# Kernel optimization log

Measured on AMD Instinct MI355X. Metric: run time of the kernel, lower is better.

Reference implementation:

```python
import jax, jax.numpy as jnp
import numpy as np
import math


def _strided_value_mask(L, S, dtype):
    # mask_line[L + d] == 0 when |d| is a power-of-two stride in {2,4,...,<=L};
    # value_mask[i, j] = mask_line[L - i + j], i.e. zero where |j - i| is such a stride.
    diff = jnp.abs(jnp.arange(L)[:, None] - jnp.arange(S)[None, :])  # [L, S]
    vm = jnp.ones((L, S), dtype=dtype)
    stride = 2
    while stride <= L:
        vm = vm * (diff != stride).astype(dtype)
        stride *= 2
    return vm


def setup_inputs() -> dict:
    key = jax.random.key(0)
    k1, k2, k3 = jax.random.split(key, 3)
    B, L, H, E = 4, 2048, 8, 64
    D = 64
    return {
        "queries": jax.random.normal(k1, (B, L, H, E), dtype=jnp.float32),
        "keys": jax.random.normal(k2, (B, L, H, E), dtype=jnp.float32),
        "values": jax.random.normal(k3, (B, L, H, D), dtype=jnp.float32),
    }


def reference(queries, keys, values):
    B, L, H, E = queries.shape
    S = keys.shape[1]
    scale = 1.0 / math.sqrt(E)

    # raw scores [B, H, L, S]
    scores = jnp.einsum("blhe,bshe->bhls", queries, keys)
    # multiplicative strided mask (zeroes scores at power-of-two offsets)
    vm = _strided_value_mask(L, S, scores.dtype)  # [L, S]
    scores = scores * vm
    # causal mask: upper triangle -> -inf (mask_flag=True, attn_mask=None path)
    causal = jnp.triu(jnp.ones((L, S), dtype=bool), k=1)
    scores = jnp.where(causal, -jnp.inf, scores)

    # dropout p=0.0 (eval) -> identity
    A = jax.nn.softmax(scale * scores, axis=-1)
    V = jnp.einsum("bhls,bshd->blhd", A, values)
    return V
```

## Files before the change

### kernel.cpp

```cpp
#include <hip/hip_runtime.h>
#include <hip/hip_bf16.h>
#include <stdint.h>

typedef __attribute__((ext_vector_type(8))) short short8;
typedef __attribute__((ext_vector_type(16))) float f32x16;

namespace {
constexpr int NB = 4, NL = 2048, NH = 8, NE = 64, ND = 64;
constexpr float KS = 0.125f * 1.44269504f;
constexpr int NCHUNK = 40;
constexpr int RECSZ  = 8320;
constexpr int KSTEP  = 64 * NH * NE;
}

__device__ const unsigned char TG[40] = {
  3,7,7,10,11,11,11,14,14,15,15,15,15,
  6,6,9,9,10,10,12,12,13,13,13,13,14,14,
  2,5,5,8,8,8,9,12,12,
  4,4,1,0};
__device__ const unsigned char TT0[40] = {
  0,0,16,0,0,16,32,0,16,0,16,32,48,
  0,14,0,14,16,30,0,14,0,14,28,42,32,46,
  0,0,12,0,12,24,28,28,40,
  0,10,0,0};
__device__ const unsigned char TT1[40] = {
  16,16,32,16,16,32,48,16,32,16,32,48,64,
  14,28,14,28,30,44,14,28,14,28,42,56,46,60,
  12,12,24,12,24,36,40,40,52,
  10,20,8,4};
__device__ const unsigned char TREC[40] = {
  3,10,11,18,21,22,23,32,33,36,37,38,39,
  8,9,15,16,19,20,24,25,28,29,30,31,34,35,
  2,6,7,12,13,14,17,26,27,
  4,5,1,0};
__device__ const unsigned char CUMD[16] = {0,1,2,3,4,6,8,10,12,15,18,21,24,28,32,36};
__device__ const unsigned char NCHD[16] = {1,1,1,1,2,2,2,2,3,3,3,3,4,4,4,4};

__device__ __forceinline__ ushort bfb(float x) {
  __hip_bfloat16 b(x);
  return __builtin_bit_cast(ushort, b);
}
__device__ __forceinline__ uint32_t pkbf(float lo, float hi) {
  return (uint32_t)bfb(lo) | ((uint32_t)bfb(hi) << 16);
}

#define LD(RR) do {                                                         \
    const float* kp_ = kpp + (size_t)(RR) * KSTEP;                          \
    const float* vp_ = vpp + (size_t)(RR) * KSTEP;                          \
    kx0 = *(const float4*)(kp_);      kx1 = *(const float4*)(kp_ + 4);      \
    kx2 = *(const float4*)(kp_ + 8);  kx3 = *(const float4*)(kp_ + 12);     \
    vx0 = *(const float4*)(vp_);               vx1 = *(const float4*)(vp_ + NH*ND); \
    vx2 = *(const float4*)(vp_ + 2*NH*ND);     vx3 = *(const float4*)(vp_ + 3*NH*ND); \
  } while (0)

#define STG() do {                                                          \
    uint4 kwA = { pkbf(kx0.x,kx0.y), pkbf(kx0.z,kx0.w),                     \
                  pkbf(kx1.x,kx1.y), pkbf(kx1.z,kx1.w) };                   \
    uint4 kwB = { pkbf(kx2.x,kx2.y), pkbf(kx2.z,kx2.w),                     \
                  pkbf(kx3.x,kx3.y), pkbf(kx3.z,kx3.w) };                   \
    *(uint4*)((char*)lds.kt + krow*128 + ( kcol2        ^ kswz)) = kwA;     \
    *(uint4*)((char*)lds.kt + krow*128 + ((kcol2 + 16)  ^ kswz)) = kwB;     \
    _Pragma("unroll")                                                       \
    for (int j_ = 0; j_ < 4; ++j_) {                                        \
      int d_ = vd0 + j_;                                                    \
      char* vr_ = (char*)lds.vt + d_*128;                                   \
      int vs_ = (d_ & 7) << 4;                                              \
      *(uint32_t*)(vr_ + ((vk0*2    ) ^ vs_)) = pkbf(vx0[j_], vx1[j_]);     \
      *(uint32_t*)(vr_ + ((vk0*2 + 4) ^ vs_)) = pkbf(vx2[j_], vx3[j_]);     \
    }                                                                       \
  } while (0)

#define COMPUTE(TT, SUB) do {                                               \
    const int kv0_ = (TT) * 32;                                             \
    f32x16 s;                                                               \
    _Pragma("unroll")                                                       \
    for (int i_ = 0; i_ < 16; ++i_) s[i_] = 0.f;                            \
    { const char* kb_ = (const char*)lds.kt + ((SUB)*32 + ln31) * 128;      \
      _Pragma("unroll")                                                     \
      for (int st_ = 0; st_ < 4; ++st_) {                                   \
        short8 kf_ = *(const short8*)(kb_ + ((st_*32 + hi*16) ^ rsw));      \
        s = __builtin_amdgcn_mfma_f32_32x32x16_bf16(kf_, qf[st_], s, 0,0,0);\
      } }                                                                   \
    const int delta_ = q0w - kv0_;                                          \
    const int qrelh_ = (qi - kv0_) - 4 * hi;                                \
    if ((TT) == tw) {                          \
      _Pragma("unroll")                                                     \
      for (int r_ = 0; r_ < 16; ++r_) {                                     \
        const int cr_ = (r_ & 3) + 8 * (r_ >> 2);                           \
        int diff_ = qrelh_ - cr_;                                           \
        float lg_ = s[r_];                                                  \
        bool p2_ = (diff_ > 1) & ((diff_ & (diff_ - 1)) == 0);              \
        lg_ = p2_ ? 0.f : lg_;                                              \
        lg_ = (diff_ < 0) ? -__builtin_inff() : lg_;                        \
        s[r_] = exp2f(lg_);                                                 \
      }                                                                     \
    } else {                                                                \
      int pmax_ = 1 << (31 - __clz(delta_ + 31));                           \
      if (pmax_ >= delta_ - 31) {        \
        _Pragma("unroll")                                                   \
        for (int r_ = 0; r_ < 16; ++r_) {                                   \
          const int cr_ = (r_ & 3) + 8 * (r_ >> 2);                         \
          int diff_ = qrelh_ - cr_;                                         \
          bool p2_ = (diff_ > 1) & ((diff_ & (diff_ - 1)) == 0);            \
          s[r_] = exp2f(p2_ ? 0.f : s[r_]);                                 \
        }                                                                   \
      } else {                                        \
        _Pragma("unroll")                                                   \
        for (int r_ = 0; r_ < 16; ++r_) s[r_] = exp2f(s[r_]);               \
      }                                                                     \
    }                                                                       \
    uint32_t w0_ = pkbf(s[0],  s[1]),  w1_ = pkbf(s[2],  s[3]);             \
    uint32_t w2_ = pkbf(s[4],  s[5]),  w3_ = pkbf(s[6],  s[7]);             \
    uint32_t w4_ = pkbf(s[8],  s[9]),  w5_ = pkbf(s[10], s[11]);            \
    uint32_t w6_ = pkbf(s[12], s[13]), w7_ = pkbf(s[14], s[15]);            \
    uint32_t y0_ = __shfl_xor(hi ? w0_ : w2_, 32);                          \
    uint32_t y1_ = __shfl_xor(hi ? w1_ : w3_, 32);                          \
    uint32_t y2_ = __shfl_xor(hi ? w4_ : w6_, 32);                          \
    uint32_t y3_ = __shfl_xor(hi ? w5_ : w7_, 32);                          \
    union { short8 v; uint32_t u[4]; } f0_, f1_;                            \
    if (hi == 0) {                                                          \
      f0_.u[0] = w0_; f0_.u[1] = w1_; f0_.u[2] = y0_; f0_.u[3] = y1_;       \
      f1_.u[0] = w4_; f1_.u[1] = w5_; f1_.u[2] = y2_; f1_.u[3] = y3_;       \
    } else {                                                                \
      f0_.u[0] = y0_; f0_.u[1] = y1_; f0_.u[2] = w2_; f0_.u[3] = w3_;       \
      f1_.u[0] = y2_; f1_.u[1] = y3_; f1_.u[2] = w6_; f1_.u[3] = w7_;       \
    }                                                                       \
    { const char* vb_ = (const char*)lds.vt;                                \
      const char* vr0_ = vb_ + ln31 * 128;                                  \
      const char* vr1_ = vb_ + (32 + ln31) * 128;                           \
      short8 a00_ = *(const short8*)(vr0_ + (((SUB)*64      + hi*16) ^ rsw));\
      short8 a01_ = *(const short8*)(vr0_ + (((SUB)*64 + 32 + hi*16) ^ rsw));\
      short8 a10_ = *(const short8*)(vr1_ + (((SUB)*64      + hi*16) ^ rsw));\
      short8 a11_ = *(const short8*)(vr1_ + (((SUB)*64 + 32 + hi*16) ^ rsw));\
      acc0 = __builtin_amdgcn_mfma_f32_32x32x16_bf16(a00_, f0_.v, acc0, 0,0,0); \
      acc0 = __builtin_amdgcn_mfma_f32_32x32x16_bf16(a01_, f1_.v, acc0, 0,0,0); \
      acc1 = __builtin_amdgcn_mfma_f32_32x32x16_bf16(a10_, f0_.v, acc1, 0,0,0); \
      acc1 = __builtin_amdgcn_mfma_f32_32x32x16_bf16(a11_, f1_.v, acc1, 0,0,0); \
      accl = __builtin_amdgcn_mfma_f32_32x32x16_bf16(onesv, f0_.v, accl, 0,0,0);\
      accl = __builtin_amdgcn_mfma_f32_32x32x16_bf16(onesv, f1_.v, accl, 0,0,0);\
    }                                                                       \
  } while (0)

__global__ __launch_bounds__(256, 3)
void sattn_part(const float* __restrict__ Qg, const float* __restrict__ Kg,
                const float* __restrict__ Vg, float* __restrict__ W)
{
  const int id = blockIdx.x;
  const int bh = id & 31;
  const int e  = id >> 5;
  const int g  = TG[e];
  const int t0 = TT0[e], t1 = TT1[e];
  float* rec = W + (size_t)(bh * NCHUNK + TREC[e]) * RECSZ;
  const int b = bh >> 3, h = bh & 7;

  const int tid  = threadIdx.x;
  const int wave = tid >> 6;
  const int lane = tid & 63;
  const int ln31 = lane & 31;
  const int hi   = lane >> 5;

  __shared__ __align__(16) struct { ushort kt[64 * 64]; ushort vt[64 * 64]; } lds;

  const int q0w = g * 128 + wave * 32;
  const int qi  = q0w + ln31;
  const int tw  = 4 * g + wave;

  short8 qf[4];
  {
    const float* qp = Qg + (((size_t)b * NL + qi) * NH + h) * NE;
    #pragma unroll
    for (int st = 0; st < 4; ++st) {
      const float* qpe = qp + st * 16 + hi * 8;
      union { short8 v; uint32_t u[4]; } f;
      #pragma unroll
      for (int j = 0; j < 4; ++j)
        f.u[j] = pkbf(qpe[2 * j] * KS, qpe[2 * j + 1] * KS);
      qf[st] = f.v;
    }
  }
  short8 onesv;
  {
    union { short8 v; uint32_t u[4]; } o;
    #pragma unroll
    for (int j = 0; j < 4; ++j) o.u[j] = 0x3F803F80u;
    onesv = o.v;
  }

  f32x16 acc0, acc1, accl;
  #pragma unroll
  for (int i = 0; i < 16; ++i) { acc0[i] = 0.f; acc1[i] = 0.f; accl[i] = 0.f; }

  const int krow = tid >> 2,        kcol = (tid & 3) * 16;
  const int vk0  = (tid & 15) * 4,  vd0  = (tid >> 4) * 4;
  const int kbase = t0 * 32;
  const float* kpp = Kg + (((size_t)b * NL + kbase + krow) * NH + h) * NE + kcol;
  const float* vpp = Vg + (((size_t)b * NL + kbase + vk0 ) * NH + h) * ND + vd0;

  const int kswz  = (krow & 7) << 4;
  const int kcol2 = kcol * 2;
  const int rsw   = (ln31 & 7) << 4;

  float4 kx0, kx1, kx2, kx3, vx0, vx1, vx2, vx3;

  const int nr = (t1 - t0) >> 1;
  LD(0);
  STG();
  __syncthreads();
  if (nr > 1) LD(1);
  for (int r = 0;;) {
    const int tt = t0 + 2 * r;
    if (tt     <= tw) COMPUTE(tt,     0);
    if (tt + 1 <= tw) COMPUTE(tt + 1, 1);
    if (++r == nr) break;
    __syncthreads();
    STG();
    __syncthreads();
    if (r + 1 < nr) LD(r + 1);
  }

  #pragma unroll
  for (int r = 0; r < 16; ++r) {
    int d = (r & 3) + 8 * (r >> 2) + 4 * hi;
    rec[d * 128 + wave * 32 + ln31]        = acc0[r];
    rec[(32 + d) * 128 + wave * 32 + ln31] = acc1[r];
  }
  if (hi == 0) rec[8192 + wave * 32 + ln31] = accl[0];
}

__global__ __launch_bounds__(256)
void sattn_combine(const float* __restrict__ W, float* __restrict__ Og)
{
  const int id = blockIdx.x;
  const int h2 = id & 1, g = (id >> 1) & 15, bh = id >> 5;
  const int b = bh >> 3, h = bh & 7;
  const int tid = threadIdx.x;

  __shared__ float sd[64][67];
  __shared__ float Lq[64];

  const float* rec0 = W + (size_t)(bh * NCHUNK + CUMD[g]) * RECSZ;
  const int nc = NCHD[g];

  #pragma unroll
  for (int rep = 0; rep < 4; ++rep) {
    int d  = rep * 16 + (tid >> 4);
    int q4 = (tid & 15) * 4;
    float4 a = {0.f, 0.f, 0.f, 0.f};
    for (int c = 0; c < nc; ++c) {
      float4 v = *(const float4*)(rec0 + (size_t)c * RECSZ + d * 128 + h2 * 64 + q4);
      a.x += v.x; a.y += v.y; a.z += v.z; a.w += v.w;
    }
    sd[d][q4 + 0] = a.x; sd[d][q4 + 1] = a.y;
    sd[d][q4 + 2] = a.z; sd[d][q4 + 3] = a.w;
  }
  if (tid < 64) {
    float a = 0.f;
    for (int c = 0; c < nc; ++c) a += rec0[(size_t)c * RECSZ + 8192 + h2 * 64 + tid];
    Lq[tid] = 1.0f / a;
  }
  __syncthreads();
  #pragma unroll
  for (int rep = 0; rep < 4; ++rep) {
    int q  = rep * 16 + (tid >> 4);
    int d4 = (tid & 15) * 4;
    float l = Lq[q];
    float4 o = { sd[d4][q] * l, sd[d4 + 1][q] * l, sd[d4 + 2][q] * l, sd[d4 + 3][q] * l };
    *(float4*)(Og + (((size_t)b * NL + g * 128 + h2 * 64 + q) * NH + h) * ND + d4) = o;
  }
}

__global__ __launch_bounds__(256)
void sattn_mono(const float* __restrict__ Qg, const float* __restrict__ Kg,
                const float* __restrict__ Vg, float* __restrict__ Og)
{
  const int bh = blockIdx.x;
  const int y  = blockIdx.y;
  const int qblk = (y < 8) ? (15 - y) : (y - 8);
  const int b = bh >> 3, h = bh & 7;
  const int tid  = threadIdx.x;
  const int wave = tid >> 6;
  const int lane = tid & 63;
  const int ln31 = lane & 31;
  const int hi   = lane >> 5;

  __shared__ __align__(16) union {
    struct { ushort kt[32 * 64]; ushort vt[64 * 40]; } s;
    float ep[4 * 32 * 68];
  } lds;

  const int q0w = qblk * 128 + wave * 32;
  const int qi  = q0w + ln31;
  const int tw  = qblk * 4 + wave;
  const int NT  = qblk * 4 + 4;

  short8 qf[4];
  {
    const float* qp = Qg + (((size_t)b * NL + qi) * NH + h) * NE;
    #pragma unroll
    for (int st = 0; st < 4; ++st) {
      const float* qpe = qp + st * 16 + hi * 8;
      union { short8 v; uint32_t u[4]; } f;
      #pragma unroll
      for (int j = 0; j < 4; ++j) f.u[j] = pkbf(qpe[2 * j] * KS, qpe[2 * j + 1] * KS);
      qf[st] = f.v;
    }
  }
  f32x16 acc0, acc1;
  #pragma unroll
  for (int i = 0; i < 16; ++i) { acc0[i] = 0.f; acc1[i] = 0.f; }
  float ls = 0.f;

  const int krow = tid >> 3,        kcol = (tid & 7) * 8;
  const int vrow = (tid >> 4) * 2,  vcol = (tid & 15) * 4;
  const float* kpp = Kg + (((size_t)b * NL + krow) * NH + h) * NE + kcol;
  const float* vpp = Vg + (((size_t)b * NL + vrow) * NH + h) * ND + vcol;
  constexpr int KS32 = 32 * NH * NE;

  float kx[8], vx[8];
  #pragma unroll
  for (int j = 0; j < 8; ++j) kx[j] = kpp[j];
  #pragma unroll
  for (int j = 0; j < 4; ++j) { vx[j] = vpp[j]; vx[4 + j] = vpp[j + NH * ND]; }

  for (int t = 0; t < NT; ++t) {
    const int kv0 = t * 32;
    __syncthreads();
    {
      uint32_t* kd = (uint32_t*)((char*)lds.s.kt + krow * 128 +
                                 ((kcol * 2) ^ ((krow & 7) << 4)));
      kd[0] = pkbf(kx[0], kx[1]); kd[1] = pkbf(kx[2], kx[3]);
      kd[2] = pkbf(kx[4], kx[5]); kd[3] = pkbf(kx[6], kx[7]);
      #pragma unroll
      for (int j = 0; j < 4; ++j) {
        int d = vcol + j;
        *(uint32_t*)((char*)lds.s.vt + d * 80 +
                     ((vrow * 2) ^ (((d >> 3) & 3) << 4))) = pkbf(vx[j], vx[4 + j]);
      }
    }
    {
      int tn = (t + 1 < NT) ? t + 1 : t;
      const float* kp = kpp + (size_t)tn * KS32;
      const float* vp = vpp + (size_t)tn * KS32;
      #pragma unroll
      for (int j = 0; j < 8; ++j) kx[j] = kp[j];
      #pragma unroll
      for (int j = 0; j < 4; ++j) { vx[j] = vp[j]; vx[4 + j] = vp[j + NH * ND]; }
    }
    __syncthreads();
    if (t > tw) continue;

    f32x16 s;
    #pragma unroll
    for (int i = 0; i < 16; ++i) s[i] = 0.f;
    const char* kb  = (const char*)lds.s.kt + ln31 * 128;
    const int   ksw = (ln31 & 7) << 4;
    #pragma unroll
    for (int st = 0; st < 4; ++st) {
      short8 kf = *(const short8*)(kb + ((st * 32 + hi * 16) ^ ksw));
      s = __builtin_amdgcn_mfma_f32_32x32x16_bf16(kf, qf[st], s, 0, 0, 0);
    }
    const int delta = q0w - kv0;
    const int qrelh = (qi - kv0) - 4 * hi;
    float ps = 0.f;
    if (t == tw) {
      #pragma unroll
      for (int r = 0; r < 16; ++r) {
        const int cr = (r & 3) + 8 * (r >> 2);
        int diff = qrelh - cr;
        float lg = s[r];
        bool p2 = (diff > 1) & ((diff & (diff - 1)) == 0);
        lg = p2 ? 0.f : lg;
        lg = (diff < 0) ? -__builtin_inff() : lg;
        float p = exp2f(lg); s[r] = p; ps += p;
      }
    } else {
      int pmax = 1 << (31 - __clz(delta + 31));
      if (pmax >= delta - 31) {
        #pragma unroll
        for (int r = 0; r < 16; ++r) {
          const int cr = (r & 3) + 8 * (r >> 2);
          int diff = qrelh - cr;
          bool p2 = (diff > 1) & ((diff & (diff - 1)) == 0);
          float p = exp2f(p2 ? 0.f : s[r]); s[r] = p; ps += p;
        }
      } else {
        #pragma unroll
        for (int r = 0; r < 16; ++r) { float p = exp2f(s[r]); s[r] = p; ps += p; }
      }
    }
    ls += ps;

    uint32_t w0 = pkbf(s[0],  s[1]),  w1 = pkbf(s[2],  s[3]);
    uint32_t w2 = pkbf(s[4],  s[5]),  w3 = pkbf(s[6],  s[7]);
    uint32_t w4 = pkbf(s[8],  s[9]),  w5 = pkbf(s[10], s[11]);
    uint32_t w6 = pkbf(s[12], s[13]), w7 = pkbf(s[14], s[15]);
    uint32_t y0 = __shfl_xor(hi ? w0 : w2, 32);
    uint32_t y1 = __shfl_xor(hi ? w1 : w3, 32);
    uint32_t y2 = __shfl_xor(hi ? w4 : w6, 32);
    uint32_t y3 = __shfl_xor(hi ? w5 : w7, 32);
    union { short8 v; uint32_t u[4]; } f0, f1;
    if (hi == 0) {
      f0.u[0] = w0; f0.u[1] = w1; f0.u[2] = y0; f0.u[3] = y1;
      f1.u[0] = w4; f1.u[1] = w5; f1.u[2] = y2; f1.u[3] = y3;
    } else {
      f0.u[0] = y0; f0.u[1] = y1; f0.u[2] = w2; f0.u[3] = w3;
      f1.u[0] = y2; f1.u[1] = y3; f1.u[2] = w6; f1.u[3] = w7;
    }
    const char* vb = (const char*)lds.s.vt;
    const int d0 = ln31,      sw0 = ((d0 >> 3) & 3) << 4;
    const int d1 = 32 + ln31, sw1 = ((d1 >> 3) & 3) << 4;
    short8 a00 = *(const short8*)(vb + d0 * 80 + ((hi * 16) ^ sw0));
    short8 a01 = *(const short8*)(vb + d0 * 80 + ((32 + hi * 16) ^ sw0));
    short8 a10 = *(const short8*)(vb + d1 * 80 + ((hi * 16) ^ sw1));
    short8 a11 = *(const short8*)(vb + d1 * 80 + ((32 + hi * 16) ^ sw1));
    acc0 = __builtin_amdgcn_mfma_f32_32x32x16_bf16(a00, f0.v, acc0, 0, 0, 0);
    acc0 = __builtin_amdgcn_mfma_f32_32x32x16_bf16(a01, f1.v, acc0, 0, 0, 0);
    acc1 = __builtin_amdgcn_mfma_f32_32x32x16_bf16(a10, f0.v, acc1, 0, 0, 0);
    acc1 = __builtin_amdgcn_mfma_f32_32x32x16_bf16(a11, f1.v, acc1, 0, 0, 0);
  }

  __syncthreads();
  ls += __shfl_xor(ls, 32);
  const float inv = 1.0f / ls;
  float* ep = lds.ep + wave * (32 * 68);
  #pragma unroll
  for (int r = 0; r < 16; ++r) {
    int drow = (r & 3) + 8 * (r >> 2) + 4 * hi;
    ep[ln31 * 68 + drow]      = acc0[r] * inv;
    ep[ln31 * 68 + 32 + drow] = acc1[r] * inv;
  }
  __syncthreads();
  const float* epr = lds.ep + wave * (32 * 68);
  #pragma unroll
  for (int rep = 0; rep < 8; ++rep) {
    int q  = rep * 4 + (lane >> 4);
    int d4 = (lane & 15) * 4;
    float4 val = *(const float4*)(epr + q * 68 + d4);
    float* op = Og + (((size_t)b * NL + q0w + q) * NH + h) * ND + d4;
    *(float4*)op = val;
  }
}

extern "C" void kernel_launch(void* const* d_in, const int* in_sizes, int n_in,
                              void* d_out, int out_size, void* d_ws, size_t ws_size,
                              hipStream_t stream) {
  const float* Q = (const float*)d_in[0];
  const float* K = (const float*)d_in[1];
  const float* V = (const float*)d_in[2];
  float* O = (float*)d_out;
  const size_t need = (size_t)32 * NCHUNK * RECSZ * sizeof(float);
  if (ws_size >= need) {
    sattn_part<<<dim3(32 * NCHUNK), dim3(256), 0, stream>>>(Q, K, V, (float*)d_ws);
    sattn_combine<<<dim3(1024), dim3(256), 0, stream>>>((const float*)d_ws, O);
  } else {
    sattn_mono<<<dim3(32, 16), dim3(256), 0, stream>>>(Q, K, V, O);
  }
}
```

Before: 65.49 us.

## Double-buffer K/V tiles in LDS to drop one barrier per iteration

Splits the shared-memory K/V staging area into two ping-pong buffers so the next tile can be written while the current one is read. This removes one of the two __syncthreads per iteration. The global load for the next tile is now issued before compute, and the launch bound is raised to 4 blocks per CU. LDS use doubles to 32KB per block, and the added occupancy target may limit registers and cause spills.

```diff
diff --git a/kernel.cpp b/kernel.cpp
--- a/kernel.cpp
+++ b/kernel.cpp
@@ -53,29 +53,29 @@
     vx2 = *(const float4*)(vp_ + 2*NH*ND);     vx3 = *(const float4*)(vp_ + 3*NH*ND); \
   } while (0)
 
-#define STG() do {                                                          \
+#define STG(KB, VB) do {                                                    \
     uint4 kwA = { pkbf(kx0.x,kx0.y), pkbf(kx0.z,kx0.w),                     \
                   pkbf(kx1.x,kx1.y), pkbf(kx1.z,kx1.w) };                   \
     uint4 kwB = { pkbf(kx2.x,kx2.y), pkbf(kx2.z,kx2.w),                     \
                   pkbf(kx3.x,kx3.y), pkbf(kx3.z,kx3.w) };                   \
-    *(uint4*)((char*)lds.kt + krow*128 + ( kcol2        ^ kswz)) = kwA;     \
-    *(uint4*)((char*)lds.kt + krow*128 + ((kcol2 + 16)  ^ kswz)) = kwB;     \
+    *(uint4*)((KB) + krow*128 + ( kcol2        ^ kswz)) = kwA;              \
+    *(uint4*)((KB) + krow*128 + ((kcol2 + 16)  ^ kswz)) = kwB;              \
     _Pragma("unroll")                                                       \
     for (int j_ = 0; j_ < 4; ++j_) {                                        \
       int d_ = vd0 + j_;                                                    \
-      char* vr_ = (char*)lds.vt + d_*128;                                   \
+      char* vr_ = (VB) + d_*128;                                            \
       int vs_ = (d_ & 7) << 4;                                              \
       *(uint32_t*)(vr_ + ((vk0*2    ) ^ vs_)) = pkbf(vx0[j_], vx1[j_]);     \
       *(uint32_t*)(vr_ + ((vk0*2 + 4) ^ vs_)) = pkbf(vx2[j_], vx3[j_]);     \
     }                                                                       \
   } while (0)
 
-#define COMPUTE(TT, SUB) do {                                               \
+#define COMPUTE(TT, SUB, KB, VB) do {                                       \
     const int kv0_ = (TT) * 32;                                             \
     f32x16 s;                                                               \
     _Pragma("unroll")                                                       \
     for (int i_ = 0; i_ < 16; ++i_) s[i_] = 0.f;                            \
-    { const char* kb_ = (const char*)lds.kt + ((SUB)*32 + ln31) * 128;      \
+    { const char* kb_ = (const char*)(KB) + ((SUB)*32 + ln31) * 128;        \
       _Pragma("unroll")                                                     \
       for (int st_ = 0; st_ < 4; ++st_) {                                   \
         short8 kf_ = *(const short8*)(kb_ + ((st_*32 + hi*16) ^ rsw));      \
@@ -125,9 +125,8 @@
       f0_.u[0] = y0_; f0_.u[1] = y1_; f0_.u[2] = w2_; f0_.u[3] = w3_;       \
       f1_.u[0] = y2_; f1_.u[1] = y3_; f1_.u[2] = w6_; f1_.u[3] = w7_;       \
     }                                                                       \
-    { const char* vb_ = (const char*)lds.vt;                                \
-      const char* vr0_ = vb_ + ln31 * 128;                                  \
-      const char* vr1_ = vb_ + (32 + ln31) * 128;                           \
+    { const char* vr0_ = (const char*)(VB) + ln31 * 128;                    \
+      const char* vr1_ = (const char*)(VB) + (32 + ln31) * 128;             \
       short8 a00_ = *(const short8*)(vr0_ + (((SUB)*64      + hi*16) ^ rsw));\
       short8 a01_ = *(const short8*)(vr0_ + (((SUB)*64 + 32 + hi*16) ^ rsw));\
       short8 a10_ = *(const short8*)(vr1_ + (((SUB)*64      + hi*16) ^ rsw));\
@@ -141,7 +140,7 @@
     }                                                                       \
   } while (0)
 
-__global__ __launch_bounds__(256, 3)
+__global__ __launch_bounds__(256, 4)
 void sattn_part(const float* __restrict__ Qg, const float* __restrict__ Kg,
                 const float* __restrict__ Vg, float* __restrict__ W)
 {
@@ -159,7 +158,11 @@
   const int ln31 = lane & 31;
   const int hi   = lane >> 5;
 
-  __shared__ __align__(16) struct { ushort kt[64 * 64]; ushort vt[64 * 64]; } lds;
+  __shared__ __align__(16) char smem[4 * 8192];
+  char* const kbuf0 = smem;
+  char* const kbuf1 = smem + 8192;
+  char* const vbuf0 = smem + 16384;
+  char* const vbuf1 = smem + 24576;
 
   const int q0w = g * 128 + wave * 32;
   const int qi  = q0w + ln31;
@@ -204,18 +207,23 @@
 
   const int nr = (t1 - t0) >> 1;
   LD(0);
-  STG();
+  STG(kbuf0, vbuf0);
   __syncthreads();
-  if (nr > 1) LD(1);
-  for (int r = 0;;) {
+  int p = 0;
+  for (int r = 0; r < nr; ++r) {
     const int tt = t0 + 2 * r;
-    if (tt     <= tw) COMPUTE(tt,     0);
-    if (tt + 1 <= tw) COMPUTE(tt + 1, 1);
-    if (++r == nr) break;
-    __syncthreads();
-    STG();
-    __syncthreads();
+    char* kc = p ? kbuf1 : kbuf0;
+    char* vc = p ? vbuf1 : vbuf0;
     if (r + 1 < nr) LD(r + 1);
+    if (tt     <= tw) COMPUTE(tt,     0, kc, vc);
+    if (tt + 1 <= tw) COMPUTE(tt + 1, 1, kc, vc);
+    if (r + 1 < nr) {
+      char* kn = p ? kbuf0 : kbuf1;
+      char* vn = p ? vbuf0 : vbuf1;
+      STG(kn, vn);
+      __syncthreads();
+      p ^= 1;
+    }
   }
 
   #pragma unroll
```

Result: slower. 180.5 us (+175.6%).
